# Kernel tuning notes

Measured on AMD Instinct MI355X. Metric: run time of the kernel, lower is better.

The kernel has to match this reference:

```python
import jax, jax.numpy as jnp
import numpy as np

N, F, T = 128, 32, 5  # nodes, node features, time steps (time_steps=5 in module)
SCALE = 0.1           # scale uniform params so sigmoid/tanh stay non-degenerate


def setup_inputs() -> dict:
    key = jax.random.key(0)
    ks = jax.random.split(key, 10)
    node_features = jax.random.normal(ks[0], (N, F), dtype=jnp.float32)
    A = jax.random.randint(ks[1], (N, N), 0, 9) == 0
    adjacency = (A | A.T) & (~jnp.eye(N, dtype=bool))
    u = lambda k, shape: jax.random.uniform(k, shape, dtype=jnp.float32) * SCALE
    W_u = u(ks[2], (N, N, F, F))   # w_gru_update_gate_features
    U_u = u(ks[3], (N, N, F, F))   # u_gru_update_gate
    W_cm = u(ks[4], (N, N, F, F))  # w_gru_current_memory_message_features
    U_cm = u(ks[5], (N, N, F, F))  # u_gru_current_memory_message
    b_u = u(ks[6], (F,))           # b_gru_update_gate
    b_cm = u(ks[7], (F,))          # b_gru_current_memory_message
    U_nf = u(ks[8], (N, F, F))     # u_graph_node_features
    U_nm = u(ks[9], (N, F, F))     # u_graph_neighbor_messages
    return dict(node_features=node_features, adjacency=adjacency,
                W_u=W_u, U_u=U_u, W_cm=W_cm, U_cm=U_cm,
                b_u=b_u, b_cm=b_cm, U_nf=U_nf, U_nm=U_nm)


def _encode(x, Af, W_u, U_u, W_cm, U_cm, b_u, b_cm, U_nf, U_nm):
    # messages[i, j] = message on directed edge i -> j (edge_slice = (start, end))
    Am = Af[..., None]  # [N, N, 1] edge mask
    # node-feature terms do not depend on messages -> hoist out of the time loop
    Wu_x = jnp.einsum('ijfg,ig->ijf', W_u, x)    # W_u[i,j] @ x[i]
    Wcm_x = jnp.einsum('ijfg,ig->ijf', W_cm, x)  # W_cm[i,j] @ x[i]
    messages = jnp.zeros((N, N, F), dtype=x.dtype)
    for _ in range(T):
        m = messages * Am
        # prev[i,j] = sum_{k in N(i), k != j} messages[k, i]
        S_in = jnp.sum(m, axis=0)                         # [N, F], S_in[i] = sum_k m[k, i]
        prev = S_in[:, None, :] - jnp.swapaxes(m, 0, 1)   # subtract m[j, i]
        # update gate z[i,j] = sigmoid(W_u[i,j]@x_i + U_u[i,j]@prev[i,j] + b_u)
        z = jax.nn.sigmoid(Wu_x + jnp.einsum('ijfg,ijg->ijf', U_u, prev) + b_u)
        # reset gate r[i,k] (same weights as update gate, per source code):
        # r[i,k] = sigmoid(W_u[i,k]@x_i + U_u[i,k]@messages[i,k] + b_u)
        r = jax.nn.sigmoid(Wu_x + jnp.einsum('ijfg,ijg->ijf', U_u, m) + b_u)
        # reset_sum[i,j] = sum_{k in N(i), k != j} r[i,k] * messages[i,k]
        rm = r * m
        reset_sum = jnp.sum(rm, axis=1)[:, None, :] - rm
        # current memory: tanh(W_cm[i,j]@x_i + U_cm[i,j]@reset_sum[i,j] + b_cm)
        cm = jnp.tanh(Wcm_x + jnp.einsum('ijfg,ijg->ijf', U_cm, reset_sum) + b_cm)
        # GRU compose, write only on existing edges (non-edges stay zero)
        messages = ((1.0 - z) * prev + z * cm) * Am
    # node encoding: relu(U_nf[i]@x_i + U_nm[i]@sum_j messages[i, j])
    out_sum = jnp.sum(messages, axis=1)  # [N, F]
    enc = jax.nn.relu(jnp.einsum('ifg,ig->if', U_nf, x) +
                      jnp.einsum('ifg,ig->if', U_nm, out_sum))
    return enc


def reference(node_features, adjacency, W_u, U_u, W_cm, U_cm, b_u, b_cm, U_nf, U_nm):
    Af = adjacency.astype(node_features.dtype)
    return _encode(node_features, Af, W_u, U_u, W_cm, U_cm, b_u, b_cm, U_nf, U_nm)
```

## Files before the change

### kernel.cpp

```cpp
#include <hip/hip_runtime.h>
#include <math.h>

#define NN 128
#define FF 32
#define NBLK_E 896
#define GSTRIDE (NBLK_E * 4)

__device__ __forceinline__ float sig_(float v) { return 1.f / (1.f + expf(-v)); }

#define DOT4(acc, u4, vec, g0)                                         \
    acc += u4.x * __shfl(vec, (g0) + 0) + u4.y * __shfl(vec, (g0) + 1) \
         + u4.z * __shfl(vec, (g0) + 2) + u4.w * __shfl(vec, (g0) + 3);

__global__ __launch_bounds__(1024) void k_prep(
        const int* __restrict__ adj, float* __restrict__ acc,
        int* __restrict__ elist, int* __restrict__ meta) {
    const int t = threadIdx.x, lane = t & 63, wid = t >> 6;
    for (int g = t; g < 8 * NN * FF; g += 1024) acc[g] = 0.f;

    const int4* ap = (const int4*)(adj + t * 16);
    const int4 v0 = ap[0], v1 = ap[1], v2 = ap[2], v3 = ap[3];
    const int c[16] = {v0.x, v0.y, v0.z, v0.w, v1.x, v1.y, v1.z, v1.w,
                       v2.x, v2.y, v2.z, v2.w, v3.x, v3.y, v3.z, v3.w};
    int fl = 0;
#pragma unroll
    for (int k = 0; k < 16; ++k)
        if (c[k]) fl |= (1 << k);
    const int cnt = __popc(fl);

    int inc = cnt;
#pragma unroll
    for (int d = 1; d < 64; d <<= 1) {
        const int n = __shfl_up(inc, d);
        if (lane >= d) inc += n;
    }
    __shared__ int wtot[16], wbase[16], Etot_s;
    if (lane == 63) wtot[wid] = inc;
    __syncthreads();
    if (t < 16) {
        const int v = wtot[t];
        int pz = v;
#pragma unroll
        for (int d = 1; d < 16; d <<= 1) {
            const int n = __shfl_up(pz, d);
            if (t >= d) pz += n;
        }
        wbase[t] = pz - v;
        if (t == 15) Etot_s = pz;
    }
    __syncthreads();
    const int base = wbase[wid] + (inc - cnt);
    if ((t & 7) == 0) meta[1 + (t >> 3)] = base;
    if (t == 0) { meta[0] = Etot_s; meta[129] = Etot_s; }
    int off = base;
#pragma unroll
    for (int k = 0; k < 16; ++k)
        if ((fl >> k) & 1) elist[off++] = t * 16 + k;
}

__global__ __launch_bounds__(256) void k_step0(
        const int* __restrict__ elist, const int* __restrict__ meta,
        const float* __restrict__ x,
        const float* __restrict__ Wu, const float* __restrict__ Wcm,
        const float* __restrict__ Uu,
        const float* __restrict__ bu, const float* __restrict__ bcm,
        float* __restrict__ WUX, float* __restrict__ WCMX,
        float* __restrict__ M1, float* __restrict__ RM,
        float* __restrict__ sin1, float* __restrict__ rout1) {
    const int E = meta[0];
    const int gw = blockIdx.x * 4 + (threadIdx.x >> 6);
    const int l = threadIdx.x & 63;
    const int f = l >> 1, h = l & 1, ll = l & 31;
    const float bu_f = bu[f], bcm_f = bcm[f];
    for (int slot = gw; slot < E; slot += GSTRIDE) {
        const int e = elist[slot];
        const int i = e >> 7, j = e & 127;
        const size_t rb = ((size_t)e * FF + f) * FF + h * 16;
        const float xv = x[i * FF + ll];
        const float4* __restrict__ wp = (const float4*)(Wu + rb);
        const float4* __restrict__ cp = (const float4*)(Wcm + rb);
        float a0 = 0.f, a1 = 0.f;
#pragma unroll
        for (int q = 0; q < 4; ++q) {
            const float4 w4 = wp[q], c4 = cp[q];
            const int g0 = h * 16 + q * 4;
            DOT4(a0, w4, xv, g0)
            DOT4(a1, c4, xv, g0)
        }
        a0 += __shfl_xor(a0, 1);
        a1 += __shfl_xor(a1, 1);
        if (h == 0) {
            WUX[(size_t)e * FF + f] = a0;
            WCMX[(size_t)e * FF + f] = a1;
        }
        const float m_pair = sig_(a0 + bu_f) * tanhf(a1 + bcm_f);
        const float mv = __shfl(m_pair, 2 * ll);
        if (l < 32) {
            M1[(size_t)e * FF + ll] = mv;
            atomicAdd(&sin1[j * FF + ll], mv);
        }
        const float4* __restrict__ up = (const float4*)(Uu + rb);
        float aR = 0.f;
#pragma unroll
        for (int q = 0; q < 4; ++q) {
            const float4 u4 = up[q];
            const int g0 = h * 16 + q * 4;
            DOT4(aR, u4, mv, g0)
        }
        aR += __shfl_xor(aR, 1);
        const float rm_pair = sig_(a0 + aR + bu_f) * m_pair;
        const float rmv = __shfl(rm_pair, 2 * ll);
        if (l < 32) {
            RM[(size_t)e * FF + ll] = rmv;
            atomicAdd(&rout1[i * FF + ll], rmv);
        }
    }
}

__global__ __launch_bounds__(256) void k_step(
        const int* __restrict__ elist, const int* __restrict__ meta,
        const float* __restrict__ Uu, const float* __restrict__ Ucm,
        const float* __restrict__ bu, const float* __restrict__ bcm,
        const float* __restrict__ WUX, const float* __restrict__ WCMX,
        const float* __restrict__ M_in, float* __restrict__ M_out,
        float* __restrict__ RM,
        const float* __restrict__ sin_t, const float* __restrict__ rout_t,
        float* __restrict__ sin_next, float* __restrict__ rout_next) {
    const int E = meta[0];
    const int gw = blockIdx.x * 4 + (threadIdx.x >> 6);
    const int l = threadIdx.x & 63;
    const int f = l >> 1, h = l & 1, ll = l & 31;
    const float bu_f = bu[f], bcm_f = bcm[f];
    for (int slot = gw; slot < E; slot += GSTRIDE) {
        const int e = elist[slot];
        const int i = e >> 7, j = e & 127;
        const size_t rb = ((size_t)e * FF + f) * FF + h * 16;

        const float prevv = sin_t[i * FF + ll] - M_in[((size_t)j * NN + i) * FF + ll];
        const float4* __restrict__ up = (const float4*)(Uu + rb);
        const float4 u0 = up[0], u1 = up[1], u2 = up[2], u3 = up[3];
        float aP = 0.f;
        {
            const int g0 = h * 16;
            DOT4(aP, u0, prevv, g0 + 0)
            DOT4(aP, u1, prevv, g0 + 4)
            DOT4(aP, u2, prevv, g0 + 8)
            DOT4(aP, u3, prevv, g0 + 12)
        }
        aP += __shfl_xor(aP, 1);
        const float wux_f = WUX[(size_t)e * FF + f];
        const float z = sig_(wux_f + aP + bu_f);

        const float rsv = rout_t[i * FF + ll] - RM[(size_t)e * FF + ll];
        const float4* __restrict__ cp = (const float4*)(Ucm + rb);
        float aC = 0.f;
        {
            const int g0 = h * 16;
            DOT4(aC, cp[0], rsv, g0 + 0)
            DOT4(aC, cp[1], rsv, g0 + 4)
            DOT4(aC, cp[2], rsv, g0 + 8)
            DOT4(aC, cp[3], rsv, g0 + 12)
        }
        aC += __shfl_xor(aC, 1);
        const float cmv = tanhf(WCMX[(size_t)e * FF + f] + aC + bcm_f);

        const float prev_f = __shfl(prevv, f);
        const float m_pair = (1.f - z) * prev_f + z * cmv;
        const float mv = __shfl(m_pair, 2 * ll);
        if (l < 32) {
            M_out[(size_t)e * FF + ll] = mv;
            atomicAdd(&sin_next[j * FF + ll], mv);
        }
        float aR = 0.f;
        {
            const int g0 = h * 16;
            DOT4(aR, u0, mv, g0 + 0)
            DOT4(aR, u1, mv, g0 + 4)
            DOT4(aR, u2, mv, g0 + 8)
            DOT4(aR, u3, mv, g0 + 12)
        }
        aR += __shfl_xor(aR, 1);
        const float rm_pair = sig_(wux_f + aR + bu_f) * m_pair;
        const float rmv = __shfl(rm_pair, 2 * ll);
        if (l < 32) {
            RM[(size_t)e * FF + ll] = rmv;
            atomicAdd(&rout_next[i * FF + ll], rmv);
        }
    }
}

__global__ __launch_bounds__(1024) void k_last(
        const int* __restrict__ elist, const int* __restrict__ meta,
        const float* __restrict__ x,
        const float* __restrict__ Uu, const float* __restrict__ Ucm,
        const float* __restrict__ bu, const float* __restrict__ bcm,
        const float* __restrict__ WUX, const float* __restrict__ WCMX,
        const float* __restrict__ M_in, const float* __restrict__ RM,
        const float* __restrict__ sin4, const float* __restrict__ rout4,
        const float* __restrict__ Unf, const float* __restrict__ Unm,
        float* __restrict__ out) {
    const int i = blockIdx.x;
    const int t = threadIdx.x;
    const int wv = t >> 6, l = t & 63;
    const int f = l >> 1, h = l & 1, ll = l & 31;
    const int rs = meta[1 + i], re = meta[2 + i];
    const float sinv = sin4[i * FF + ll];
    const float routv = rout4[i * FF + ll];
    const float bu_f = bu[f], bcm_f = bcm[f];

    float osv = 0.f;
    for (int s = rs + wv; s < re; s += 16) {
        const int e = elist[s];
        const int j = e & 127;
        const size_t rb = ((size_t)e * FF + f) * FF + h * 16;
        const float prevv = sinv - M_in[((size_t)j * NN + i) * FF + ll];
        const float4* __restrict__ up = (const float4*)(Uu + rb);
        float aP = 0.f;
        {
            const int g0 = h * 16;
            DOT4(aP, up[0], prevv, g0 + 0)
            DOT4(aP, up[1], prevv, g0 + 4)
            DOT4(aP, up[2], prevv, g0 + 8)
            DOT4(aP, up[3], prevv, g0 + 12)
        }
        aP += __shfl_xor(aP, 1);
        const float z = sig_(WUX[(size_t)e * FF + f] + aP + bu_f);

        const float rsv = routv - RM[(size_t)e * FF + ll];
        const float4* __restrict__ cp = (const float4*)(Ucm + rb);
        float aC = 0.f;
        {
            const int g0 = h * 16;
            DOT4(aC, cp[0], rsv, g0 + 0)
            DOT4(aC, cp[1], rsv, g0 + 4)
            DOT4(aC, cp[2], rsv, g0 + 8)
            DOT4(aC, cp[3], rsv, g0 + 12)
        }
        aC += __shfl_xor(aC, 1);
        const float cmv = tanhf(WCMX[(size_t)e * FF + f] + aC + bcm_f);

        const float prev_f = __shfl(prevv, f);
        const float m_pair = (1.f - z) * prev_f + z * cmv;
        osv += __shfl(m_pair, 2 * ll);
    }
    __shared__ float opp[16][FF];
    if (l < 32) opp[wv][ll] = osv;
    __syncthreads();
    if (t < 64) {
        float os = 0.f;
#pragma unroll
        for (int g = 0; g < 16; ++g) os += opp[g][ll];
        const float xv = x[i * FF + ll];
        const size_t rb = ((size_t)i * FF + f) * FF + h * 16;
        const float4* __restrict__ fp = (const float4*)(Unf + rb);
        const float4* __restrict__ mp = (const float4*)(Unm + rb);
        float a = 0.f;
#pragma unroll
        for (int q = 0; q < 4; ++q) {
            const float4 f4 = fp[q], m4 = mp[q];
            const int g0 = h * 16 + q * 4;
            DOT4(a, f4, xv, g0)
            DOT4(a, m4, os, g0)
        }
        a += __shfl_xor(a, 1);
        if (h == 0) out[i * FF + f] = fmaxf(a, 0.f);
    }
}

extern "C" void kernel_launch(void* const* d_in, const int* in_sizes, int n_in,
                              void* d_out, int out_size, void* d_ws, size_t ws_size,
                              hipStream_t stream) {
    const float* x   = (const float*)d_in[0];
    const int*   adj = (const int*)d_in[1];
    const float* Wu  = (const float*)d_in[2];
    const float* Uu  = (const float*)d_in[3];
    const float* Wcm = (const float*)d_in[4];
    const float* Ucm = (const float*)d_in[5];
    const float* bu  = (const float*)d_in[6];
    const float* bcm = (const float*)d_in[7];
    const float* Unf = (const float*)d_in[8];
    const float* Unm = (const float*)d_in[9];
    float* out = (float*)d_out;

    const size_t EF = (size_t)NN * NN * FF;
    const size_t NF = (size_t)NN * FF;
    float* p    = (float*)d_ws;
    float* MA   = p; p += EF;
    float* MB   = p; p += EF;
    float* WUX  = p; p += EF;
    float* WCMX = p; p += EF;
    float* RM   = p; p += EF;
    float* acc  = p; p += 8 * NF;
    int* elist  = (int*)p;
    int* meta   = elist + NN * NN;
    float* sinb[4]  = {acc, acc + NF, acc + 2 * NF, acc + 3 * NF};
    float* routb[4] = {acc + 4 * NF, acc + 5 * NF, acc + 6 * NF, acc + 7 * NF};

    k_prep<<<1, 1024, 0, stream>>>(adj, acc, elist, meta);
    k_step0<<<NBLK_E, 256, 0, stream>>>(elist, meta, x, Wu, Wcm, Uu, bu, bcm,
                                        WUX, WCMX, MA, RM, sinb[0], routb[0]);
    k_step<<<NBLK_E, 256, 0, stream>>>(elist, meta, Uu, Ucm, bu, bcm, WUX, WCMX,
                                       MA, MB, RM, sinb[0], routb[0],
                                       sinb[1], routb[1]);
    k_step<<<NBLK_E, 256, 0, stream>>>(elist, meta, Uu, Ucm, bu, bcm, WUX, WCMX,
                                       MB, MA, RM, sinb[1], routb[1],
                                       sinb[2], routb[2]);
    k_step<<<NBLK_E, 256, 0, stream>>>(elist, meta, Uu, Ucm, bu, bcm, WUX, WCMX,
                                       MA, MB, RM, sinb[2], routb[2],
                                       sinb[3], routb[3]);
    k_last<<<NN, 1024, 0, stream>>>(elist, meta, x, Uu, Ucm, bu, bcm,
                                    WUX, WCMX, MB, RM, sinb[3], routb[3],
                                    Unf, Unm, out);
}
```

Before: 50.14 us.

## Replace edge-list compaction and atomic reductions with dense-grid per-edge neighbor gathers

Drops the single-block edge-list prep kernel and the atomic scatter of per-node sums. Each step kernel now launches one wave per (i,j) pair, exits early on non-edges, and recomputes S_in and the reset sum by ballot-scanning the adjacency row and gathering neighbor messages. The reset-message buffer is double-buffered, and the last kernel shrinks from 1024 to 256 threads per block. This removes one serial launch and the atomic contention, but adds a redundant neighbor gather of roughly degree times 32 floats per edge and many empty waves.

```diff
diff --git a/kernel.cpp b/kernel.cpp
--- a/kernel.cpp
+++ b/kernel.cpp
@@ -3,8 +3,7 @@
 
 #define NN 128
 #define FF 32
-#define NBLK_E 896
-#define GSTRIDE (NBLK_E * 4)
+#define EG ((NN * NN) / 4)
 
 __device__ __forceinline__ float sig_(float v) { return 1.f / (1.f + expf(-v)); }
 
@@ -12,244 +11,219 @@
     acc += u4.x * __shfl(vec, (g0) + 0) + u4.y * __shfl(vec, (g0) + 1) \
          + u4.z * __shfl(vec, (g0) + 2) + u4.w * __shfl(vec, (g0) + 3);
 
-__global__ __launch_bounds__(1024) void k_prep(
-        const int* __restrict__ adj, float* __restrict__ acc,
-        int* __restrict__ elist, int* __restrict__ meta) {
-    const int t = threadIdx.x, lane = t & 63, wid = t >> 6;
-    for (int g = t; g < 8 * NN * FF; g += 1024) acc[g] = 0.f;
-
-    const int4* ap = (const int4*)(adj + t * 16);
-    const int4 v0 = ap[0], v1 = ap[1], v2 = ap[2], v3 = ap[3];
-    const int c[16] = {v0.x, v0.y, v0.z, v0.w, v1.x, v1.y, v1.z, v1.w,
-                       v2.x, v2.y, v2.z, v2.w, v3.x, v3.y, v3.z, v3.w};
-    int fl = 0;
-#pragma unroll
-    for (int k = 0; k < 16; ++k)
-        if (c[k]) fl |= (1 << k);
-    const int cnt = __popc(fl);
-
-    int inc = cnt;
-#pragma unroll
-    for (int d = 1; d < 64; d <<= 1) {
-        const int n = __shfl_up(inc, d);
-        if (lane >= d) inc += n;
-    }
-    __shared__ int wtot[16], wbase[16], Etot_s;
-    if (lane == 63) wtot[wid] = inc;
-    __syncthreads();
-    if (t < 16) {
-        const int v = wtot[t];
-        int pz = v;
-#pragma unroll
-        for (int d = 1; d < 16; d <<= 1) {
-            const int n = __shfl_up(pz, d);
-            if (t >= d) pz += n;
-        }
-        wbase[t] = pz - v;
-        if (t == 15) Etot_s = pz;
-    }
-    __syncthreads();
-    const int base = wbase[wid] + (inc - cnt);
-    if ((t & 7) == 0) meta[1 + (t >> 3)] = base;
-    if (t == 0) { meta[0] = Etot_s; meta[129] = Etot_s; }
-    int off = base;
-#pragma unroll
-    for (int k = 0; k < 16; ++k)
-        if ((fl >> k) & 1) elist[off++] = t * 16 + k;
-}
-
 __global__ __launch_bounds__(256) void k_step0(
-        const int* __restrict__ elist, const int* __restrict__ meta,
-        const float* __restrict__ x,
+        const int* __restrict__ adj, const float* __restrict__ x,
         const float* __restrict__ Wu, const float* __restrict__ Wcm,
         const float* __restrict__ Uu,
         const float* __restrict__ bu, const float* __restrict__ bcm,
         float* __restrict__ WUX, float* __restrict__ WCMX,
-        float* __restrict__ M1, float* __restrict__ RM,
-        float* __restrict__ sin1, float* __restrict__ rout1) {
-    const int E = meta[0];
-    const int gw = blockIdx.x * 4 + (threadIdx.x >> 6);
+        float* __restrict__ M1, float* __restrict__ RM1) {
+    const int e = blockIdx.x * 4 + (threadIdx.x >> 6);
+    if (!adj[e]) return;
     const int l = threadIdx.x & 63;
+    const int i = e >> 7;
     const int f = l >> 1, h = l & 1, ll = l & 31;
     const float bu_f = bu[f], bcm_f = bcm[f];
-    for (int slot = gw; slot < E; slot += GSTRIDE) {
-        const int e = elist[slot];
-        const int i = e >> 7, j = e & 127;
-        const size_t rb = ((size_t)e * FF + f) * FF + h * 16;
-        const float xv = x[i * FF + ll];
-        const float4* __restrict__ wp = (const float4*)(Wu + rb);
-        const float4* __restrict__ cp = (const float4*)(Wcm + rb);
-        float a0 = 0.f, a1 = 0.f;
-#pragma unroll
-        for (int q = 0; q < 4; ++q) {
-            const float4 w4 = wp[q], c4 = cp[q];
-            const int g0 = h * 16 + q * 4;
-            DOT4(a0, w4, xv, g0)
-            DOT4(a1, c4, xv, g0)
-        }
-        a0 += __shfl_xor(a0, 1);
-        a1 += __shfl_xor(a1, 1);
-        if (h == 0) {
-            WUX[(size_t)e * FF + f] = a0;
-            WCMX[(size_t)e * FF + f] = a1;
-        }
-        const float m_pair = sig_(a0 + bu_f) * tanhf(a1 + bcm_f);
-        const float mv = __shfl(m_pair, 2 * ll);
-        if (l < 32) {
-            M1[(size_t)e * FF + ll] = mv;
-            atomicAdd(&sin1[j * FF + ll], mv);
-        }
-        const float4* __restrict__ up = (const float4*)(Uu + rb);
-        float aR = 0.f;
-#pragma unroll
-        for (int q = 0; q < 4; ++q) {
-            const float4 u4 = up[q];
-            const int g0 = h * 16 + q * 4;
-            DOT4(aR, u4, mv, g0)
-        }
-        aR += __shfl_xor(aR, 1);
-        const float rm_pair = sig_(a0 + aR + bu_f) * m_pair;
-        const float rmv = __shfl(rm_pair, 2 * ll);
-        if (l < 32) {
-            RM[(size_t)e * FF + ll] = rmv;
-            atomicAdd(&rout1[i * FF + ll], rmv);
-        }
-    }
+    const size_t rb = ((size_t)e * FF + f) * FF + h * 16;
+    const float xv = x[i * FF + ll];
+    const float4* __restrict__ wp = (const float4*)(Wu + rb);
+    const float4* __restrict__ cp = (const float4*)(Wcm + rb);
+    float a0 = 0.f, a1 = 0.f;
+#pragma unroll
+    for (int q = 0; q < 4; ++q) {
+        const float4 w4 = wp[q], c4 = cp[q];
+        const int g0 = h * 16 + q * 4;
+        DOT4(a0, w4, xv, g0)
+        DOT4(a1, c4, xv, g0)
+    }
+    a0 += __shfl_xor(a0, 1);
+    a1 += __shfl_xor(a1, 1);
+    if (h == 0) {
+        WUX[(size_t)e * FF + f] = a0;
+        WCMX[(size_t)e * FF + f] = a1;
+    }
+    const float m_pair = sig_(a0 + bu_f) * tanhf(a1 + bcm_f);
+    const float mv = __shfl(m_pair, 2 * ll);
+    if (l < 32) M1[(size_t)e * FF + ll] = mv;
+    const float4* __restrict__ up = (const float4*)(Uu + rb);
+    float aR = 0.f;
+#pragma unroll
+    for (int q = 0; q < 4; ++q) {
+        const float4 u4 = up[q];
+        const int g0 = h * 16 + q * 4;
+        DOT4(aR, u4, mv, g0)
+    }
+    aR += __shfl_xor(aR, 1);
+    const float rm_pair = sig_(a0 + aR + bu_f) * m_pair;
+    const float rmv = __shfl(rm_pair, 2 * ll);
+    if (l < 32) RM1[(size_t)e * FF + ll] = rmv;
 }
 
 __global__ __launch_bounds__(256) void k_step(
-        const int* __restrict__ elist, const int* __restrict__ meta,
+        const int* __restrict__ adj,
         const float* __restrict__ Uu, const float* __restrict__ Ucm,
         const float* __restrict__ bu, const float* __restrict__ bcm,
         const float* __restrict__ WUX, const float* __restrict__ WCMX,
         const float* __restrict__ M_in, float* __restrict__ M_out,
-        float* __restrict__ RM,
-        const float* __restrict__ sin_t, const float* __restrict__ rout_t,
-        float* __restrict__ sin_next, float* __restrict__ rout_next) {
-    const int E = meta[0];
-    const int gw = blockIdx.x * 4 + (threadIdx.x >> 6);
+        const float* __restrict__ RM_in, float* __restrict__ RM_out) {
+    const int e = blockIdx.x * 4 + (threadIdx.x >> 6);
+    if (!adj[e]) return;
     const int l = threadIdx.x & 63;
+    const int i = e >> 7, j = e & 127;
     const int f = l >> 1, h = l & 1, ll = l & 31;
     const float bu_f = bu[f], bcm_f = bcm[f];
-    for (int slot = gw; slot < E; slot += GSTRIDE) {
-        const int e = elist[slot];
-        const int i = e >> 7, j = e & 127;
-        const size_t rb = ((size_t)e * FF + f) * FF + h * 16;
-
-        const float prevv = sin_t[i * FF + ll] - M_in[((size_t)j * NN + i) * FF + ll];
-        const float4* __restrict__ up = (const float4*)(Uu + rb);
-        const float4 u0 = up[0], u1 = up[1], u2 = up[2], u3 = up[3];
-        float aP = 0.f;
-        {
-            const int g0 = h * 16;
-            DOT4(aP, u0, prevv, g0 + 0)
-            DOT4(aP, u1, prevv, g0 + 4)
-            DOT4(aP, u2, prevv, g0 + 8)
-            DOT4(aP, u3, prevv, g0 + 12)
-        }
-        aP += __shfl_xor(aP, 1);
-        const float wux_f = WUX[(size_t)e * FF + f];
-        const float z = sig_(wux_f + aP + bu_f);
-
-        const float rsv = rout_t[i * FF + ll] - RM[(size_t)e * FF + ll];
-        const float4* __restrict__ cp = (const float4*)(Ucm + rb);
-        float aC = 0.f;
-        {
-            const int g0 = h * 16;
-            DOT4(aC, cp[0], rsv, g0 + 0)
-            DOT4(aC, cp[1], rsv, g0 + 4)
-            DOT4(aC, cp[2], rsv, g0 + 8)
-            DOT4(aC, cp[3], rsv, g0 + 12)
-        }
-        aC += __shfl_xor(aC, 1);
-        const float cmv = tanhf(WCMX[(size_t)e * FF + f] + aC + bcm_f);
-
-        const float prev_f = __shfl(prevv, f);
-        const float m_pair = (1.f - z) * prev_f + z * cmv;
-        const float mv = __shfl(m_pair, 2 * ll);
-        if (l < 32) {
-            M_out[(size_t)e * FF + ll] = mv;
-            atomicAdd(&sin_next[j * FF + ll], mv);
-        }
-        float aR = 0.f;
-        {
-            const int g0 = h * 16;
-            DOT4(aR, u0, mv, g0 + 0)
-            DOT4(aR, u1, mv, g0 + 4)
-            DOT4(aR, u2, mv, g0 + 8)
-            DOT4(aR, u3, mv, g0 + 12)
-        }
-        aR += __shfl_xor(aR, 1);
-        const float rm_pair = sig_(wux_f + aR + bu_f) * m_pair;
-        const float rmv = __shfl(rm_pair, 2 * ll);
-        if (l < 32) {
-            RM[(size_t)e * FF + ll] = rmv;
-            atomicAdd(&rout_next[i * FF + ll], rmv);
-        }
-    }
-}
-
-__global__ __launch_bounds__(1024) void k_last(
-        const int* __restrict__ elist, const int* __restrict__ meta,
-        const float* __restrict__ x,
+    const size_t rb = ((size_t)e * FF + f) * FF + h * 16;
+
+    const unsigned long long mlo = __ballot(adj[i * NN + l] != 0);
+    const unsigned long long mhi = __ballot(adj[i * NN + 64 + l] != 0);
+
+    float sinv = 0.f, routv = 0.f;
+    {
+        unsigned long long m = mlo;
+        while (m) {
+            const int k = __ffsll(m) - 1; m &= m - 1;
+            sinv  += M_in[((size_t)k * NN + i) * FF + ll];
+            routv += RM_in[((size_t)i * NN + k) * FF + ll];
+        }
+        m = mhi;
+        while (m) {
+            const int k = __ffsll(m) - 1 + 64; m &= m - 1;
+            sinv  += M_in[((size_t)k * NN + i) * FF + ll];
+            routv += RM_in[((size_t)i * NN + k) * FF + ll];
+        }
+    }
+
+    const float prevv = sinv - M_in[((size_t)j * NN + i) * FF + ll];
+    const float4* __restrict__ up = (const float4*)(Uu + rb);
+    const float4 u0 = up[0], u1 = up[1], u2 = up[2], u3 = up[3];
+    float aP = 0.f;
+    {
+        const int g0 = h * 16;
+        DOT4(aP, u0, prevv, g0 + 0)
+        DOT4(aP, u1, prevv, g0 + 4)
+        DOT4(aP, u2, prevv, g0 + 8)
+        DOT4(aP, u3, prevv, g0 + 12)
+    }
+    aP += __shfl_xor(aP, 1);
+    const float wux_f = WUX[(size_t)e * FF + f];
+    const float z = sig_(wux_f + aP + bu_f);
+
+    const float rsv = routv - RM_in[(size_t)e * FF + ll];
+    const float4* __restrict__ cp = (const float4*)(Ucm + rb);
+    float aC = 0.f;
+    {
+        const int g0 = h * 16;
+        DOT4(aC, cp[0], rsv, g0 + 0)
+        DOT4(aC, cp[1], rsv, g0 + 4)
+        DOT4(aC, cp[2], rsv, g0 + 8)
+        DOT4(aC, cp[3], rsv, g0 + 12)
+    }
+    aC += __shfl_xor(aC, 1);
+    const float cmv = tanhf(WCMX[(size_t)e * FF + f] + aC + bcm_f);
+
+    const float prev_f = __shfl(prevv, f);
+    const float m_pair = (1.f - z) * prev_f + z * cmv;
+    const float mv = __shfl(m_pair, 2 * ll);
+    if (l < 32) M_out[(size_t)e * FF + ll] = mv;
+
+    float aR = 0.f;
+    {
+        const int g0 = h * 16;
+        DOT4(aR, u0, mv, g0 + 0)
+        DOT4(aR, u1, mv, g0 + 4)
+        DOT4(aR, u2, mv, g0 + 8)
+        DOT4(aR, u3, mv, g0 + 12)
+    }
+    aR += __shfl_xor(aR, 1);
+    const float rm_pair = sig_(wux_f + aR + bu_f) * m_pair;
+    const float rmv = __shfl(rm_pair, 2 * ll);
+    if (l < 32) RM_out[(size_t)e * FF + ll] = rmv;
+}
+
+__global__ __launch_bounds__(256) void k_last(
+        const int* __restrict__ adj, const float* __restrict__ x,
         const float* __restrict__ Uu, const float* __restrict__ Ucm,
         const float* __restrict__ bu, const float* __restrict__ bcm,
         const float* __restrict__ WUX, const float* __restrict__ WCMX,
-        const float* __restrict__ M_in, const float* __restrict__ RM,
-        const float* __restrict__ sin4, const float* __restrict__ rout4,
+        const float* __restrict__ M_in, const float* __restrict__ RM_in,
         const float* __restrict__ Unf, const float* __restrict__ Unm,
         float* __restrict__ out) {
+    __shared__ float opp[4][FF];
     const int i = blockIdx.x;
     const int t = threadIdx.x;
     const int wv = t >> 6, l = t & 63;
     const int f = l >> 1, h = l & 1, ll = l & 31;
-    const int rs = meta[1 + i], re = meta[2 + i];
-    const float sinv = sin4[i * FF + ll];
-    const float routv = rout4[i * FF + ll];
     const float bu_f = bu[f], bcm_f = bcm[f];
 
+    const unsigned long long mlo = __ballot(adj[i * NN + l] != 0);
+    const unsigned long long mhi = __ballot(adj[i * NN + 64 + l] != 0);
+
+    float sinv = 0.f, routv = 0.f;
+    {
+        unsigned long long m = mlo;
+        while (m) {
+            const int k = __ffsll(m) - 1; m &= m - 1;
+            sinv  += M_in[((size_t)k * NN + i) * FF + ll];
+            routv += RM_in[((size_t)i * NN + k) * FF + ll];
+        }
+        m = mhi;
+        while (m) {
+            const int k = __ffsll(m) - 1 + 64; m &= m - 1;
+            sinv  += M_in[((size_t)k * NN + i) * FF + ll];
+            routv += RM_in[((size_t)i * NN + k) * FF + ll];
+        }
+    }
+
     float osv = 0.f;
-    for (int s = rs + wv; s < re; s += 16) {
-        const int e = elist[s];
-        const int j = e & 127;
-        const size_t rb = ((size_t)e * FF + f) * FF + h * 16;
-        const float prevv = sinv - M_in[((size_t)j * NN + i) * FF + ll];
-        const float4* __restrict__ up = (const float4*)(Uu + rb);
-        float aP = 0.f;
-        {
-            const int g0 = h * 16;
-            DOT4(aP, up[0], prevv, g0 + 0)
-            DOT4(aP, up[1], prevv, g0 + 4)
-            DOT4(aP, up[2], prevv, g0 + 8)
-            DOT4(aP, up[3], prevv, g0 + 12)
-        }
-        aP += __shfl_xor(aP, 1);
-        const float z = sig_(WUX[(size_t)e * FF + f] + aP + bu_f);
-
-        const float rsv = routv - RM[(size_t)e * FF + ll];
-        const float4* __restrict__ cp = (const float4*)(Ucm + rb);
-        float aC = 0.f;
-        {
-            const int g0 = h * 16;
-            DOT4(aC, cp[0], rsv, g0 + 0)
-            DOT4(aC, cp[1], rsv, g0 + 4)
-            DOT4(aC, cp[2], rsv, g0 + 8)
-            DOT4(aC, cp[3], rsv, g0 + 12)
-        }
-        aC += __shfl_xor(aC, 1);
-        const float cmv = tanhf(WCMX[(size_t)e * FF + f] + aC + bcm_f);
-
-        const float prev_f = __shfl(prevv, f);
-        const float m_pair = (1.f - z) * prev_f + z * cmv;
-        osv += __shfl(m_pair, 2 * ll);
-    }
-    __shared__ float opp[16][FF];
+    int idx = 0;
+    unsigned long long m = mlo;
+#pragma unroll 1
+    for (int half = 0; half < 2; ++half) {
+        while (m) {
+            const int k = __ffsll(m) - 1 + half * 64; m &= m - 1;
+            if ((idx++ & 3) != wv) continue;
+            const int j = k;
+            const size_t e = (size_t)i * NN + j;
+            const size_t rb = (e * FF + f) * FF + h * 16;
+            const float prevv = sinv - M_in[((size_t)j * NN + i) * FF + ll];
+            const float4* __restrict__ up = (const float4*)(Uu + rb);
+            float aP = 0.f;
+            {
+                const int g0 = h * 16;
+                DOT4(aP, up[0], prevv, g0 + 0)
+                DOT4(aP, up[1], prevv, g0 + 4)
+                DOT4(aP, up[2], prevv, g0 + 8)
+                DOT4(aP, up[3], prevv, g0 + 12)
+            }
+            aP += __shfl_xor(aP, 1);
+            const float z = sig_(WUX[e * FF + f] + aP + bu_f);
+
+            const float rsv = routv - RM_in[e * FF + ll];
+            const float4* __restrict__ cp = (const float4*)(Ucm + rb);
+            float aC = 0.f;
+            {
+                const int g0 = h * 16;
+                DOT4(aC, cp[0], rsv, g0 + 0)
+                DOT4(aC, cp[1], rsv, g0 + 4)
+                DOT4(aC, cp[2], rsv, g0 + 8)
+                DOT4(aC, cp[3], rsv, g0 + 12)
+            }
+            aC += __shfl_xor(aC, 1);
+            const float cmv = tanhf(WCMX[e * FF + f] + aC + bcm_f);
+
+            const float prev_f = __shfl(prevv, f);
+            const float m_pair = (1.f - z) * prev_f + z * cmv;
+            osv += __shfl(m_pair, 2 * ll);
+        }
+        m = mhi;
+    }
+
     if (l < 32) opp[wv][ll] = osv;
     __syncthreads();
     if (t < 64) {
         float os = 0.f;
 #pragma unroll
-        for (int g = 0; g < 16; ++g) os += opp[g][ll];
+        for (int g = 0; g < 4; ++g) os += opp[g][ll];
         const float xv = x[i * FF + ll];
         const size_t rb = ((size_t)i * FF + f) * FF + h * 16;
         const float4* __restrict__ fp = (const float4*)(Unf + rb);
@@ -283,32 +257,22 @@
     float* out = (float*)d_out;
 
     const size_t EF = (size_t)NN * NN * FF;
-    const size_t NF = (size_t)NN * FF;
     float* p    = (float*)d_ws;
     float* MA   = p; p += EF;
     float* MB   = p; p += EF;
+    float* RMA  = p; p += EF;
+    float* RMB  = p; p += EF;
     float* WUX  = p; p += EF;
     float* WCMX = p; p += EF;
-    float* RM   = p; p += EF;
-    float* acc  = p; p += 8 * NF;
-    int* elist  = (int*)p;
-    int* meta   = elist + NN * NN;
-    float* sinb[4]  = {acc, acc + NF, acc + 2 * NF, acc + 3 * NF};
-    float* routb[4] = {acc + 4 * NF, acc + 5 * NF, acc + 6 * NF, acc + 7 * NF};
-
-    k_prep<<<1, 1024, 0, stream>>>(adj, acc, elist, meta);
-    k_step0<<<NBLK_E, 256, 0, stream>>>(elist, meta, x, Wu, Wcm, Uu, bu, bcm,
-                                        WUX, WCMX, MA, RM, sinb[0], routb[0]);
-    k_step<<<NBLK_E, 256, 0, stream>>>(elist, meta, Uu, Ucm, bu, bcm, WUX, WCMX,
-                                       MA, MB, RM, sinb[0], routb[0],
-                                       sinb[1], routb[1]);
-    k_step<<<NBLK_E, 256, 0, stream>>>(elist, meta, Uu, Ucm, bu, bcm, WUX, WCMX,
-                                       MB, MA, RM, sinb[1], routb[1],
-                                       sinb[2], routb[2]);
-    k_step<<<NBLK_E, 256, 0, stream>>>(elist, meta, Uu, Ucm, bu, bcm, WUX, WCMX,
-                                       MA, MB, RM, sinb[2], routb[2],
-                                       sinb[3], routb[3]);
-    k_last<<<NN, 1024, 0, stream>>>(elist, meta, x, Uu, Ucm, bu, bcm,
-                                    WUX, WCMX, MB, RM, sinb[3], routb[3],
-                                    Unf, Unm, out);
-}
+
+    k_step0<<<EG, 256, 0, stream>>>(adj, x, Wu, Wcm, Uu, bu, bcm,
+                                    WUX, WCMX, MA, RMA);
+    k_step<<<EG, 256, 0, stream>>>(adj, Uu, Ucm, bu, bcm, WUX, WCMX,
+                                   MA, MB, RMA, RMB);
+    k_step<<<EG, 256, 0, stream>>>(adj, Uu, Ucm, bu, bcm, WUX, WCMX,
+                                   MB, MA, RMB, RMA);
+    k_step<<<EG, 256, 0, stream>>>(adj, Uu, Ucm, bu, bcm, WUX, WCMX,
+                                   MA, MB, RMA, RMB);
+    k_last<<<NN, 256, 0, stream>>>(adj, x, Uu, Ucm, bu, bcm, WUX, WCMX,
+                                   MB, RMB, Unf, Unm, out);
+}
```

Measured after the change: 83.57 us. 1.67x slower.
